# Kernel optimization log

Hardware: AMD Instinct MI355X
Metric: run time of the kernel (lower is better)

## Reference

```python
import jax, jax.numpy as jnp
import numpy as np
from jax import lax

DIM = 192
HEADS = 8
B, H, W = 8, 128, 128


def dwconv3x3(x, w):
    # x: [B,C,H,W], w: [C,1,3,3] depthwise (groups=C)
    return lax.conv_general_dilated(
        x, w, window_strides=(1, 1), padding='SAME',
        feature_group_count=x.shape[1],
        dimension_numbers=('NCHW', 'OIHW', 'NCHW'))


def conv1x1(x, w, b=None):
    # w: [Cout, Cin]
    y = jnp.einsum('oc,bchw->bohw', w, x)
    if b is not None:
        y = y + b[None, :, None, None]
    return y


def setup_inputs() -> dict:
    key = jax.random.key(0)
    ks = jax.random.split(key, 9)
    s = 0.02
    return {
        'x': jax.random.normal(ks[0], (B, DIM, H, W), jnp.float32),
        'w_qkv': jax.random.normal(ks[1], (3 * DIM, DIM), jnp.float32) * s,
        'b_qkv': jnp.zeros((3 * DIM,), jnp.float32),
        'w_dw': jax.random.normal(ks[2], (3 * DIM, 1, 3, 3), jnp.float32) * s,
        'b_dw': jnp.zeros((3 * DIM,), jnp.float32),
        'w_proj': jax.random.normal(ks[3], (DIM, DIM), jnp.float32) * s,
        'b_proj': jnp.zeros((DIM,), jnp.float32),
        'w_pos1': jax.random.normal(ks[4], (DIM, 1, 3, 3), jnp.float32) * s,
        'w_pos2': jax.random.normal(ks[5], (DIM, 1, 3, 3), jnp.float32) * s,
        'temperature': jnp.ones((HEADS, 1, 1), jnp.float32),
    }


def reference(x, w_qkv, b_qkv, w_dw, b_dw, w_proj, b_proj, w_pos1, w_pos2, temperature):
    b, c, h, w = x.shape
    heads = HEADS
    ch = c // heads

    qkv = conv1x1(x, w_qkv, b_qkv)
    qkv = dwconv3x3(qkv, w_dw) + b_dw[None, :, None, None]
    q_inp, k_inp, v_inp = jnp.split(qkv, 3, axis=1)

    def to_heads(t):  # [B,C,H,W] -> [B,heads,ch,HW]
        return t.reshape(b, heads, ch, h * w)

    q = to_heads(q_inp)
    k = to_heads(k_inp)
    v = to_heads(v_inp)

    # L2 normalize over hw (torch F.normalize, eps=1e-12)
    q = q / jnp.maximum(jnp.linalg.norm(q, axis=-1, keepdims=True), 1e-12)
    k = k / jnp.maximum(jnp.linalg.norm(k, axis=-1, keepdims=True), 1e-12)

    attn = jnp.einsum('bhce,bhde->bhcd', q, k) * temperature  # [B,heads,ch,ch]
    attn = jax.nn.softmax(attn, axis=-1)
    out = jnp.einsum('bhcd,bhde->bhce', attn, v)  # [B,heads,ch,HW]
    out = out.reshape(b, c, h, w)

    out = conv1x1(out, w_proj, b_proj)

    pos = dwconv3x3(v_inp, w_pos1)
    pos = jax.nn.gelu(pos, approximate=False)
    pos = dwconv3x3(pos, w_pos2)

    return out + pos
```

## Files before the change

### kernel.cpp

```cpp
#include <hip/hip_runtime.h>
#include <stdint.h>
#include <stddef.h>

#define NB 8
#define CC 192
#define C3 576
#define HGT 128
#define WID 128
#define HW 16384
#define NH 8
#define QKROW 49152

typedef short bf16x8 __attribute__((ext_vector_type(8)));
typedef float f32x4 __attribute__((ext_vector_type(4)));

__device__ __forceinline__ unsigned short f2bf(float f) {
  unsigned int u = __float_as_uint(f);
  u += 0x7fffu + ((u >> 16) & 1u);
  return (unsigned short)(u >> 16);
}
__device__ __forceinline__ float bf2f(unsigned short h) {
  return __uint_as_float(((unsigned int)h) << 16);
}
__device__ __forceinline__ float bflo(unsigned int v) {
  return __uint_as_float(v << 16);
}
__device__ __forceinline__ float bfhi(unsigned int v) {
  return __uint_as_float(v & 0xffff0000u);
}
__device__ __forceinline__ unsigned int pk2(float a, float b) {
  return (unsigned int)f2bf(a) | ((unsigned int)f2bf(b) << 16);
}
__device__ __forceinline__ void gl_lds16(const void* g, void* l) {
  __builtin_amdgcn_global_load_lds(
      (const __attribute__((address_space(1))) unsigned int*)(uintptr_t)g,
      (__attribute__((address_space(3))) unsigned int*)(uint32_t)(uintptr_t)l,
      16, 0, 0);
}
__device__ __forceinline__ int xcd_swz(int g, int n) {
  return (g & 7) * (n >> 3) + (g >> 3);
}

__global__ void kwprep(const float* __restrict__ wq, unsigned char* __restrict__ wb) {
  int f = blockIdx.x * 256 + threadIdx.x;
  if (f >= C3 * 24) return;
  int oc = f / 24, s = f % 24;
  unsigned int wv[4];
#pragma unroll
  for (int j = 0; j < 4; ++j)
    wv[j] = pk2(wq[oc * 192 + s * 8 + 2 * j], wq[oc * 192 + s * 8 + 2 * j + 1]);
  uint4 st; st.x = wv[0]; st.y = wv[1]; st.z = wv[2]; st.w = wv[3];
  *(uint4*)(wb + (size_t)oc * 384 + ((s ^ (oc & 7)) * 16)) = st;
}

__global__ __launch_bounds__(256) void kqkv(const float* __restrict__ x,
                                            const unsigned char* __restrict__ wb,
                                            const float* __restrict__ bqkv,
                                            unsigned short* __restrict__ vout,
                                            unsigned char* __restrict__ qkout) {
  __shared__ __align__(16) unsigned char lds[81920];
  const int ABF = 49152;
  const int TRO = 73728;
  int wg = xcd_swz(blockIdx.x, gridDim.x);
  int t = wg & 255, b = wg >> 8;
  int p0 = t * 64;
  int tid = threadIdx.x;

  const unsigned char* gx = (const unsigned char*)(x + (size_t)b * CC * HW + p0);
#pragma unroll
  for (int i = 0; i < 12; ++i) {
    int f = i * 256 + tid;
    int ch = f >> 4, seg = f & 15;
    gl_lds16(gx + ((size_t)ch * HW + seg * 4) * 4, lds + f * 16);
  }
  asm volatile("s_waitcnt vmcnt(0)" ::: "memory");
  __syncthreads();
  {
    const float* lx = (const float*)lds;
    int p = tid & 63, sg = tid >> 6;
#pragma unroll
    for (int s6 = 0; s6 < 6; ++s6) {
      int s = sg * 6 + s6;
      unsigned int wv[4];
#pragma unroll
      for (int j = 0; j < 4; ++j)
        wv[j] = pk2(lx[(s * 8 + 2 * j) * 64 + p], lx[(s * 8 + 2 * j + 1) * 64 + p]);
      uint4 st; st.x = wv[0]; st.y = wv[1]; st.z = wv[2]; st.w = wv[3];
      *(uint4*)(lds + ABF + (s * 64 + p) * 16) = st;
    }
  }
  __syncthreads();

#pragma unroll
  for (int i = 0; i < 6; ++i)
    gl_lds16(wb + i * 4096 + tid * 16, lds + i * 4096 + tid * 16);

  int lane = tid & 63, w = tid >> 6;
  int l15 = lane & 15, gq = lane >> 4;
  int pw = w * 16;
  int y = t >> 1, xh = (t & 1) * 8;
  int unitw = w * 2 + (gq >> 1);
  int sub8 = (gq & 1) * 8;
  int s4 = w * 4 + gq;
  int ru = tid >> 5, rc0 = tid & 31;
  int vc = tid >> 2, vxq = tid & 3;

  for (int ot = 0; ot < 9; ++ot) {
    if (ot == 0) { asm volatile("s_waitcnt vmcnt(0)" ::: "memory"); }
    else         { asm volatile("s_waitcnt vmcnt(2)" ::: "memory"); }
    __builtin_amdgcn_s_barrier();
    __builtin_amdgcn_sched_barrier(0);
    int nb = ot & 1;
    float bias[4];
#pragma unroll
    for (int nf = 0; nf < 4; ++nf) bias[nf] = bqkv[ot * 64 + nf * 16 + l15];
    if (ot < 8) {
      const unsigned char* gB = wb + (size_t)(ot + 1) * 24576;
#pragma unroll
      for (int i = 0; i < 6; ++i)
        gl_lds16(gB + i * 4096 + tid * 16, lds + (nb ^ 1) * 24576 + i * 4096 + tid * 16);
    }
    f32x4 acc[4];
#pragma unroll
    for (int nf = 0; nf < 4; ++nf) acc[nf] = (f32x4){0.f, 0.f, 0.f, 0.f};
#pragma unroll
    for (int kk = 0; kk < 6; ++kk) {
      bf16x8 a = *(const bf16x8*)(lds + ABF + (((kk * 4 + gq) * 64) + pw + l15) * 16);
      int cb = kk * 64 + gq * 16;
#pragma unroll
      for (int nf = 0; nf < 4; ++nf) {
        int r = nf * 16 + l15;
        bf16x8 bfr = *(const bf16x8*)(lds + nb * 24576 + r * 384 + (cb ^ ((r & 7) << 4)));
        acc[nf] = __builtin_amdgcn_mfma_f32_16x16x32_bf16(a, bfr, acc[nf], 0, 0, 0);
      }
    }
    bool isq = (ot < 6);
    if (isq) {
#pragma unroll
      for (int nf = 0; nf < 4; ++nf) {
        int c = nf * 16 + l15;
        uint2 st;
        st.x = pk2(acc[nf][0] + bias[nf], acc[nf][1] + bias[nf]);
        st.y = pk2(acc[nf][2] + bias[nf], acc[nf][3] + bias[nf]);
        *(uint2*)(lds + TRO + c * 128 + ((unitw ^ (c & 7)) * 16) + sub8) = st;
      }
    } else {
#pragma unroll
      for (int nf = 0; nf < 4; ++nf) {
        int c = nf * 16 + l15;
        uint2 st;
        st.x = pk2(acc[nf][0] + bias[nf], acc[nf][1] + bias[nf]);
        st.y = pk2(acc[nf][2] + bias[nf], acc[nf][3] + bias[nf]);
        *(uint2*)(lds + TRO + c * 128 + ((s4 ^ (c & 15)) * 8)) = st;
      }
    }
    asm volatile("s_waitcnt lgkmcnt(0)" ::: "memory");
    __builtin_amdgcn_s_barrier();
    __builtin_amdgcn_sched_barrier(0);
    if (isq) {
      int part = ot / 3, cm0 = (ot % 3) * 64;
      int c1 = rc0 + 32;
      uint4 v0 = *(const uint4*)(lds + TRO + rc0 * 128 + ((ru ^ (rc0 & 7)) * 16));
      uint4 v1 = *(const uint4*)(lds + TRO + c1 * 128 + ((ru ^ (c1 & 7)) * 16));
      unsigned char* grow = qkout + ((size_t)((part * 8 + b) * 128 + y)) * QKROW +
                            (xh + ru) * 3072 + cm0 * 16;
      *(uint4*)(grow + rc0 * 16) = v0;
      *(uint4*)(grow + c1 * 16) = v1;
    } else {
      uint2 q0 = *(const uint2*)(lds + TRO + vc * 128 + (((4 * vxq + 0) ^ (vc & 15)) * 8));
      uint2 q1 = *(const uint2*)(lds + TRO + vc * 128 + (((4 * vxq + 1) ^ (vc & 15)) * 8));
      uint2 q2 = *(const uint2*)(lds + TRO + vc * 128 + (((4 * vxq + 2) ^ (vc & 15)) * 8));
      uint2 q3 = *(const uint2*)(lds + TRO + vc * 128 + (((4 * vxq + 3) ^ (vc & 15)) * 8));
      unsigned short* vp = vout + ((size_t)(b * CC + (ot - 6) * 64 + vc)) * HW + p0 + vxq * 16;
      uint4 s0; s0.x = q0.x; s0.y = q0.y; s0.z = q1.x; s0.w = q1.y;
      uint4 s1; s1.x = q2.x; s1.y = q2.y; s1.z = q3.x; s1.w = q3.y;
      *(uint4*)vp = s0;
      *(uint4*)(vp + 8) = s1;
    }
  }
}

__global__ __launch_bounds__(256) void kqk(const unsigned char* __restrict__ qk,
                                           const float* __restrict__ wdw,
                                           const float* __restrict__ bdw,
                                           float* __restrict__ G,
                                           float* __restrict__ nq,
                                           float* __restrict__ nk) {
  __shared__ __align__(16) unsigned char lds[81920];
  const int FB = 49152;
  int wg = xcd_swz(blockIdx.x, gridDim.x);
  int band = wg & 63, h = (wg >> 6) & 7, b = wg >> 9;
  int y0 = band * 2;
  int tid = threadIdx.x;
#pragma unroll
  for (int i = 0; i < 12; ++i) {
    int f = i * 256 + tid;
    int p = f / 1536, rem = f % 1536;
    int r = rem / 384, unit = rem % 384;
    int uc = unit / 24, ch = unit % 24;
    int y = y0 - 1 + r;
    if (y >= 0 && y < HGT)
      gl_lds16(qk + ((size_t)((p * 8 + b) * 128 + y)) * QKROW + uc * 3072 + (h * 24 + ch) * 16,
               lds + f * 16);
    else
      *(uint4*)(lds + f * 16) = (uint4){0, 0, 0, 0};
  }
  asm volatile("s_waitcnt vmcnt(0)" ::: "memory");
  __syncthreads();

  int lane = tid & 63, w = tid >> 6;
  if (tid < 192) {
    int p = tid / 96; int r3m = tid % 96;
    int ch = r3m >> 2; int row = (r3m >> 1) & 1; int half = r3m & 1;
    int gc = p * 192 + h * 24 + ch;
    float wv[9];
#pragma unroll
    for (int j = 0; j < 9; ++j) wv[j] = wdw[gc * 9 + j];
    float bias = bdw[gc];
    const unsigned char* sbase = lds + p * 24576 + ch * 16;
    unsigned char* fb = lds + FB + p * 16384 + ch * 16;
    int h8 = half * 8;
    unsigned int W[3][16];
#define LOADU(dy_, m_, u_) { \
    uint4 tt = ((u_) >= 0 && (u_) < 16) \
        ? *(const uint4*)(sbase + (row + (dy_)) * 6144 + (u_) * 384) \
        : (uint4){0, 0, 0, 0}; \
    W[dy_][(m_) * 4 + 0] = tt.x; W[dy_][(m_) * 4 + 1] = tt.y; \
    W[dy_][(m_) * 4 + 2] = tt.z; W[dy_][(m_) * 4 + 3] = tt.w; }
#pragma unroll
    for (int dy = 0; dy < 3; ++dy) {
#pragma unroll
      for (int m = 0; m < 4; ++m) { LOADU(dy, m, h8 - 1 + m); }
    }
    float nsum = 0.f;
#pragma unroll
    for (int c4 = 0; c4 < 4; ++c4) {
      if (c4 > 0) {
#pragma unroll
        for (int dy = 0; dy < 3; ++dy) {
#pragma unroll
          for (int e = 0; e < 8; ++e) W[dy][e] = W[dy][8 + e];
          LOADU(dy, 2, h8 - 1 + c4 * 2 + 2);
          LOADU(dy, 3, h8 - 1 + c4 * 2 + 3);
        }
      }
      float acc[16];
#pragma unroll
      for (int j = 0; j < 16; ++j) acc[j] = bias;
#pragma unroll
      for (int dy = 0; dy < 3; ++dy) {
        float f[18];
#pragma unroll
        for (int t2 = 0; t2 < 18; ++t2) {
          int rel = 7 + t2;
          unsigned int v = W[dy][rel >> 1];
          f[t2] = (rel & 1) ? bfhi(v) : bflo(v);
        }
#pragma unroll
        for (int j = 0; j < 16; ++j)
          acc[j] += f[j] * wv[dy * 3] + f[j + 1] * wv[dy * 3 + 1] + f[j + 2] * wv[dy * 3 + 2];
      }
#pragma unroll
      for (int j = 0; j < 16; ++j) nsum += acc[j] * acc[j];
      unsigned int pk[8];
#pragma unroll
      for (int e = 0; e < 8; ++e) pk[e] = pk2(acc[2 * e], acc[2 * e + 1]);
      int kt = row * 4 + half * 2 + (c4 >> 1);
      int gb = (c4 & 1) * 2;
      uint4 s0; s0.x = pk[0]; s0.y = pk[1]; s0.z = pk[2]; s0.w = pk[3];
      uint4 s1; s1.x = pk[4]; s1.y = pk[5]; s1.z = pk[6]; s1.w = pk[7];
      *(uint4*)(fb + kt * 2048 + gb * 512) = s0;
      *(uint4*)(fb + kt * 2048 + (gb + 1) * 512) = s1;
    }
#undef LOADU
    nsum += __shfl_xor(nsum, 1);
    nsum += __shfl_xor(nsum, 2);
    if ((tid & 3) == 0) {
      float* dst = (p == 0) ? nq : nk;
      atomicAdd(dst + (b * NH + h) * 24 + ch, nsum);
    }
  } else {
    int t2 = tid - 192;
#pragma unroll
    for (int i = 0; i < 8; ++i) {
      int f = i * 64 + t2;
      int ch8 = f & 7, gq4 = (f >> 3) & 3, kt8 = (f >> 5) & 7, pp = f >> 8;
      *(uint4*)(lds + FB + pp * 16384 + kt8 * 2048 + gq4 * 512 + (24 + ch8) * 16) =
          (uint4){0, 0, 0, 0};
    }
  }
  __syncthreads();

  int l15 = lane & 15, gq = lane >> 4;
  f32x4 acc2[2][2];
#pragma unroll
  for (int ct = 0; ct < 2; ++ct)
#pragma unroll
    for (int dt = 0; dt < 2; ++dt) acc2[ct][dt] = (f32x4){0.f, 0.f, 0.f, 0.f};
#pragma unroll
  for (int t2 = 0; t2 < 2; ++t2) {
    int kt = w * 2 + t2;
    bf16x8 aq[2], bk[2];
#pragma unroll
    for (int ct = 0; ct < 2; ++ct) {
      aq[ct] = *(const bf16x8*)(lds + FB + kt * 2048 + gq * 512 + (ct * 16 + l15) * 16);
      bk[ct] = *(const bf16x8*)(lds + FB + 16384 + kt * 2048 + gq * 512 + (ct * 16 + l15) * 16);
    }
#pragma unroll
    for (int ct = 0; ct < 2; ++ct)
#pragma unroll
      for (int dt = 0; dt < 2; ++dt)
        acc2[ct][dt] = __builtin_amdgcn_mfma_f32_16x16x32_bf16(aq[ct], bk[dt], acc2[ct][dt], 0, 0, 0);
  }
  float* gp = (float*)lds;
#pragma unroll
  for (int ct = 0; ct < 2; ++ct)
#pragma unroll
    for (int dt = 0; dt < 2; ++dt)
      *(f32x4*)(gp + (((w * 4 + ct * 2 + dt) * 64) + lane) * 4) = acc2[ct][dt];
  __syncthreads();
  float* Gb = G + (size_t)(b * NH + h) * 576;
#pragma unroll
  for (int ii = 0; ii < 3; ++ii) {
    int f = ii * 256 + tid;
    if (f < 576) {
      int c = f / 24, d = f % 24;
      int t4 = ((c >> 4) << 1) + (d >> 4);
      int lane16 = (d & 15) + (((c & 15) >> 2) << 4);
      int reg = c & 3;
      float s = 0.f;
#pragma unroll
      for (int w4 = 0; w4 < 4; ++w4)
        s += gp[((w4 * 4 + t4) * 64 + lane16) * 4 + reg];
      atomicAdd(Gb + f, s);
    }
  }
}

__global__ __launch_bounds__(256) void kdwv(const unsigned short* __restrict__ src,
                                            const float* __restrict__ wdw,
                                            const float* __restrict__ bdw,
                                            unsigned char* __restrict__ vT) {
  __shared__ __align__(16) unsigned int smem[8 * 721];
  int wg = xcd_swz(blockIdx.x, gridDim.x);
  int cg = wg % 24, rt = (wg / 24) & 15, b = wg / 384;
  int y0 = rt * 8, chg0 = cg * 8;
  int tid = threadIdx.x;
  for (int i = tid; i < 5768; i += 256) smem[i] = 0;
  __syncthreads();
#pragma unroll
  for (int i = 0; i < 5; ++i) {
    int f = i * 256 + tid;
    int ch = f / 160, rem = f % 160;
    int r = rem >> 4, seg = rem & 15;
    int y = y0 - 1 + r;
    if (y >= 0 && y < HGT) {
      uint4 v = *(const uint4*)(src + ((size_t)(b * CC + chg0 + ch)) * HW + y * WID + seg * 8);
      unsigned int* dp = smem + ch * 721 + r * 72 + 4 + seg * 4;
      dp[0] = v.x; dp[1] = v.y; dp[2] = v.z; dp[3] = v.w;
    }
  }
  __syncthreads();
  int ch = tid >> 5, u = tid & 31;
  int row = u >> 2, xs = (u & 3) * 32;
  int gch = 384 + chg0 + ch;
  float wv[9];
#pragma unroll
  for (int j = 0; j < 9; ++j) wv[j] = wdw[gch * 9 + j];
  float bias = bdw[gch];
  float outv[32];
  const unsigned int* tb = smem + ch * 721;
#pragma unroll
  for (int g = 0; g < 4; ++g) {
    int x0 = xs + g * 8;
    float v[3][12];
#pragma unroll
    for (int dy = 0; dy < 3; ++dy) {
      const unsigned int* rp = tb + (row + dy) * 72 + ((x0 + 6) >> 1);
#pragma unroll
      for (int m = 0; m < 6; ++m) {
        unsigned int w2 = rp[m];
        v[dy][2 * m] = bf2f((unsigned short)(w2 & 0xffff));
        v[dy][2 * m + 1] = bf2f((unsigned short)(w2 >> 16));
      }
    }
#pragma unroll
    for (int j = 0; j < 8; ++j) {
      float a = bias;
#pragma unroll
      for (int dy = 0; dy < 3; ++dy)
#pragma unroll
        for (int dx = 0; dx < 3; ++dx)
          a += v[dy][j + dx + 1] * wv[dy * 3 + dx];
      outv[g * 8 + j] = a;
    }
  }
  __syncthreads();
  unsigned short* vt = (unsigned short*)smem;
#pragma unroll
  for (int g = 0; g < 4; ++g)
#pragma unroll
    for (int j = 0; j < 8; j += 2) {
      int x = xs + g * 8 + j;
      ((unsigned int*)smem)[ch * 512 + row * 64 + (x >> 1)] =
          pk2(outv[g * 8 + j], outv[g * 8 + j + 1]);
    }
  __syncthreads();
#pragma unroll
  for (int i = 0; i < 4; ++i) {
    int f = i * 256 + tid;
    int r = f >> 7, col = f & 127;
    unsigned int wvp[4];
#pragma unroll
    for (int e = 0; e < 4; ++e) {
      unsigned short a = vt[(2 * e) * 1024 + r * 128 + col];
      unsigned short bb = vt[(2 * e + 1) * 1024 + r * 128 + col];
      wvp[e] = (unsigned int)a | ((unsigned int)bb << 16);
    }
    uint4 st; st.x = wvp[0]; st.y = wvp[1]; st.z = wvp[2]; st.w = wvp[3];
    *(uint4*)(vT + (((size_t)(b * 24 + cg)) * HW + (size_t)(y0 + r) * WID + col) * 16) = st;
  }
}

__global__ __launch_bounds__(256) void kattn(const float* __restrict__ G,
                                             const float* __restrict__ nq,
                                             const float* __restrict__ nk,
                                             const float* __restrict__ temp,
                                             const float* __restrict__ wproj,
                                             unsigned char* __restrict__ W2) {
  __shared__ float attn[24][24];
  __shared__ float iq[24], ik[24];
  int bh = blockIdx.x;
  int h = bh & 7, b = bh >> 3;
  int tid = threadIdx.x;
  const float* Gb = G + (size_t)bh * 576;
  if (tid < 24) { float n = sqrtf(nq[bh * 24 + tid]); iq[tid] = 1.f / fmaxf(n, 1e-12f); }
  else if (tid < 48) { float n = sqrtf(nk[bh * 24 + tid - 24]); ik[tid - 24] = 1.f / fmaxf(n, 1e-12f); }
  __syncthreads();
  if (tid < 24) {
    float tmp = temp[h];
    float row[24];
    float mx = -1e30f;
#pragma unroll
    for (int d = 0; d < 24; ++d) {
      row[d] = Gb[tid * 24 + d] * iq[tid] * ik[d] * tmp;
      mx = fmaxf(mx, row[d]);
    }
    float sum = 0.f;
#pragma unroll
    for (int d = 0; d < 24; ++d) { float e = expf(row[d] - mx); row[d] = e; sum += e; }
    float inv = 1.f / sum;
#pragma unroll
    for (int d = 0; d < 24; ++d) attn[tid][d] = row[d] * inv;
  }
  __syncthreads();
  for (int i = 0; i < 18; ++i) {
    int f = tid + i * 256;
    if (f >= 4608) break;
    int oc = f / 24, d = f % 24;
    float s = 0.f;
#pragma unroll
    for (int c = 0; c < 24; ++c) s += wproj[oc * 192 + h * 24 + c] * attn[c][d];
    int gg = h * 24 + d;
    *(unsigned short*)(W2 + ((size_t)b * CC + oc) * 384 + ((gg * 2) ^ ((oc & 7) << 4))) = f2bf(s);
  }
}

__global__ __launch_bounds__(256) void kpos(const unsigned char* __restrict__ vT,
                                            const float* __restrict__ w1,
                                            const float* __restrict__ w2,
                                            unsigned short* __restrict__ pos) {
  __shared__ unsigned int vbuf[8 * 865];
  __shared__ unsigned int d1[8 * 721];
  int wg = xcd_swz(blockIdx.x, gridDim.x);
  int cg = wg % 24, rt = (wg / 24) & 15, b = wg / 384;
  int y0 = rt * 8, g0 = cg * 8;
  int tid = threadIdx.x;
  for (int i = tid; i < 6920; i += 256) vbuf[i] = 0;
  __syncthreads();
#pragma unroll
  for (int i = 0; i < 3; ++i) {
    int f = i * 256 + tid;
    int r = f >> 6, colp = f & 63;
    int y = y0 - 2 + r;
    if (y >= 0 && y < HGT) {
      const unsigned char* base = vT + (((size_t)(b * 24 + cg)) * HW + (size_t)y * WID + colp * 2) * 16;
      uint4 va = *(const uint4*)(base);
      uint4 vb2 = *(const uint4*)(base + 16);
      unsigned int la[4] = {va.x, va.y, va.z, va.w};
      unsigned int lb[4] = {vb2.x, vb2.y, vb2.z, vb2.w};
#pragma unroll
      for (int e = 0; e < 8; ++e) {
        unsigned int a16 = (la[e >> 1] >> ((e & 1) * 16)) & 0xffff;
        unsigned int b16 = (lb[e >> 1] >> ((e & 1) * 16)) & 0xffff;
        vbuf[e * 865 + r * 72 + colp + 4] = a16 | (b16 << 16);
      }
    }
  }
  __syncthreads();
  int ch = tid >> 5, u = tid & 31;
  {
    const float* wp = w1 + (g0 + ch) * 9;
    float wl[9];
#pragma unroll
    for (int j = 0; j < 9; ++j) wl[j] = wp[j];
    int x0 = u * 4;
    for (int rr = 0; rr < 10; ++rr) {
      int y = y0 - 1 + rr;
      unsigned int o0 = 0, o1 = 0;
      if (y >= 0 && y < HGT) {
        float v[3][8];
#pragma unroll
        for (int dy = 0; dy < 3; ++dy) {
          const unsigned int* rp = vbuf + ch * 865 + (rr + dy) * 72 + ((x0 + 6) >> 1);
#pragma unroll
          for (int m = 0; m < 4; ++m) {
            unsigned int w2r = rp[m];
            v[dy][2 * m] = bf2f((unsigned short)(w2r & 0xffff));
            v[dy][2 * m + 1] = bf2f((unsigned short)(w2r >> 16));
          }
        }
        float g4[4];
#pragma unroll
        for (int j = 0; j < 4; ++j) {
          float a = 0.f;
#pragma unroll
          for (int dy = 0; dy < 3; ++dy)
#pragma unroll
            for (int dx = 0; dx < 3; ++dx)
              a += v[dy][j + dx + 1] * wl[dy * 3 + dx];
          g4[j] = 0.5f * a * (1.f + erff(a * 0.70710678118f));
        }
        o0 = pk2(g4[0], g4[1]);
        o1 = pk2(g4[2], g4[3]);
      }
      unsigned int* dp = d1 + ch * 721 + rr * 72 + ((x0 + 8) >> 1);
      dp[0] = o0; dp[1] = o1;
    }
  }
  if (tid < 160) {
    int ech = tid / 20, rem = tid % 20;
    int rr = rem >> 1, side = rem & 1;
    int x = side ? 128 : -1;
    int y = y0 - 1 + rr;
    unsigned short val = 0;
    if (y >= 0 && y < HGT) {
      const float* wp = w1 + (g0 + ech) * 9;
      float a = 0.f;
      const unsigned short* vb16 = (const unsigned short*)(vbuf + ech * 865);
#pragma unroll
      for (int dy = 0; dy < 3; ++dy)
#pragma unroll
        for (int dx = 0; dx < 3; ++dx)
          a += bf2f(vb16[(rr + dy) * 144 + (x + dx + 7)]) * wp[dy * 3 + dx];
      val = f2bf(0.5f * a * (1.f + erff(a * 0.70710678118f)));
    }
    ((unsigned short*)(d1 + ech * 721))[rr * 144 + (x + 8)] = val;
  }
  __syncthreads();
  {
    const float* wp = w2 + (g0 + ch) * 9;
    float wl[9];
#pragma unroll
    for (int j = 0; j < 9; ++j) wl[j] = wp[j];
    int row = u >> 2, xs = (u & 3) * 32;
    size_t rb = ((size_t)(b * CC + g0 + ch)) * HW + (size_t)(y0 + row) * WID;
#pragma unroll
    for (int g = 0; g < 4; ++g) {
      int x0 = xs + g * 8;
      float v[3][12];
#pragma unroll
      for (int dy = 0; dy < 3; ++dy) {
        const unsigned int* rp = d1 + ch * 721 + (row + dy) * 72 + ((x0 + 6) >> 1);
#pragma unroll
        for (int m = 0; m < 6; ++m) {
          unsigned int w2r = rp[m];
          v[dy][2 * m] = bf2f((unsigned short)(w2r & 0xffff));
          v[dy][2 * m + 1] = bf2f((unsigned short)(w2r >> 16));
        }
      }
      uint4 st;
      float o[8];
#pragma unroll
      for (int j = 0; j < 8; ++j) {
        float a = 0.f;
#pragma unroll
        for (int dy = 0; dy < 3; ++dy)
#pragma unroll
          for (int dx = 0; dx < 3; ++dx)
            a += v[dy][j + dx + 1] * wl[dy * 3 + dx];
        o[j] = a;
      }
      st.x = pk2(o[0], o[1]); st.y = pk2(o[2], o[3]);
      st.z = pk2(o[4], o[5]); st.w = pk2(o[6], o[7]);
      *(uint4*)(pos + rb + x0) = st;
    }
  }
}

__global__ __launch_bounds__(256) void kproj(const unsigned char* __restrict__ vT,
                                             const unsigned char* __restrict__ W2,
                                             const float* __restrict__ bproj,
                                             const unsigned short* __restrict__ pos,
                                             float* __restrict__ out) {
  __shared__ __align__(16) unsigned char lds[73728];
  int wg = xcd_swz(blockIdx.x, gridDim.x);
  int ot = wg % 3; int rest = wg / 3; int grp = rest & 63; int b = rest >> 6;
  int tid = threadIdx.x;
  const unsigned char* gB = W2 + ((size_t)(b * 192 + ot * 64)) * 384;
#pragma unroll
  for (int i = 0; i < 6; ++i)
    gl_lds16(gB + i * 4096 + tid * 16, lds + 49152 + i * 4096 + tid * 16);
  const unsigned char* gA = vT + (size_t)b * 24 * HW * 16;
  int t0 = grp * 4;
  {
    int p0 = t0 * 64;
#pragma unroll
    for (int i = 0; i < 6; ++i) {
      int f = i * 256 + tid;
      gl_lds16(gA + (((size_t)(f >> 6)) * HW + p0 + (f & 63)) * 16, lds + f * 16);
    }
  }
  int lane = tid & 63, w = tid >> 6;
  int l15 = lane & 15, gq = lane >> 4;
  int pw = w * 16;
  float bias[4];
  size_t obase[4];
#pragma unroll
  for (int nf = 0; nf < 4; ++nf) {
    int oc = ot * 64 + nf * 16 + l15;
    bias[nf] = bproj[oc];
    obase[nf] = ((size_t)(b * 192 + oc)) * HW;
  }
  for (int it = 0; it < 4; ++it) {
    int tile = t0 + it;
    asm volatile("s_waitcnt vmcnt(0)" ::: "memory");
    __syncthreads();
    int nb = it & 1;
    if (it < 3) {
      int p1 = (tile + 1) * 64;
#pragma unroll
      for (int i = 0; i < 6; ++i) {
        int f = i * 256 + tid;
        gl_lds16(gA + (((size_t)(f >> 6)) * HW + p1 + (f & 63)) * 16,
                 lds + ((nb ^ 1) * 24576) + f * 16);
      }
    }
    f32x4 acc[4];
#pragma unroll
    for (int nf = 0; nf < 4; ++nf) acc[nf] = (f32x4){0.f, 0.f, 0.f, 0.f};
#pragma unroll
    for (int kk = 0; kk < 6; ++kk) {
      bf16x8 a = *(const bf16x8*)(lds + nb * 24576 + ((((kk * 4 + gq) << 6) + pw + l15) * 16));
      int cb = kk * 64 + gq * 16;
#pragma unroll
      for (int nf = 0; nf < 4; ++nf) {
        int r = nf * 16 + l15;
        bf16x8 bfr = *(const bf16x8*)(lds + 49152 + r * 384 + (cb ^ ((r & 7) << 4)));
        acc[nf] = __builtin_amdgcn_mfma_f32_16x16x32_bf16(a, bfr, acc[nf], 0, 0, 0);
      }
    }
    int p = tile * 64 + pw + gq * 4;
#pragma unroll
    for (int nf = 0; nf < 4; ++nf) {
      uint2 pv = *(const uint2*)(pos + obase[nf] + p);
      float4 o;
      o.x = acc[nf][0] + bias[nf] + bf2f((unsigned short)(pv.x & 0xffff));
      o.y = acc[nf][1] + bias[nf] + bf2f((unsigned short)(pv.x >> 16));
      o.z = acc[nf][2] + bias[nf] + bf2f((unsigned short)(pv.y & 0xffff));
      o.w = acc[nf][3] + bias[nf] + bf2f((unsigned short)(pv.y >> 16));
      *(float4*)(out + obase[nf] + p) = o;
    }
  }
}

#define OFF_W   ((size_t)0)
#define OFF_G   ((size_t)221184)
#define OFF_NQ  ((size_t)368640)
#define OFF_NK  ((size_t)374784)
#define OFF_W2  ((size_t)380928)
#define OFF_QK  ((size_t)970752)
#define OFF_V   ((size_t)101634048)
#define OFF_XT  ((size_t)151965696)

extern "C" void kernel_launch(void* const* d_in, const int* in_sizes, int n_in,
                              void* d_out, int out_size, void* d_ws, size_t ws_size,
                              hipStream_t stream) {
  const float* x     = (const float*)d_in[0];
  const float* wqkv  = (const float*)d_in[1];
  const float* bqkv  = (const float*)d_in[2];
  const float* wdw   = (const float*)d_in[3];
  const float* bdw   = (const float*)d_in[4];
  const float* wproj = (const float*)d_in[5];
  const float* bproj = (const float*)d_in[6];
  const float* wpos1 = (const float*)d_in[7];
  const float* wpos2 = (const float*)d_in[8];
  const float* temp  = (const float*)d_in[9];
  unsigned char* ws = (unsigned char*)d_ws;

  hipMemsetAsync(ws + OFF_G, 0, 147456 + 6144 + 6144, stream);
  kwprep<<<54, 256, 0, stream>>>(wqkv, ws + OFF_W);
  kqkv<<<2048, 256, 0, stream>>>(x, ws + OFF_W, bqkv,
                                 (unsigned short*)(ws + OFF_V), ws + OFF_QK);
  kqk<<<4096, 256, 0, stream>>>(ws + OFF_QK, wdw, bdw, (float*)(ws + OFF_G),
                                (float*)(ws + OFF_NQ), (float*)(ws + OFF_NK));
  kdwv<<<3072, 256, 0, stream>>>((const unsigned short*)(ws + OFF_V), wdw, bdw,
                                 ws + OFF_XT);
  kattn<<<64, 256, 0, stream>>>((const float*)(ws + OFF_G), (const float*)(ws + OFF_NQ),
                                (const float*)(ws + OFF_NK), temp, wproj, ws + OFF_W2);
  kpos<<<3072, 256, 0, stream>>>(ws + OFF_XT, wpos1, wpos2,
                                 (unsigned short*)(ws + OFF_QK));
  kproj<<<1536, 256, 0, stream>>>(ws + OFF_XT, ws + OFF_W2, bproj,
                                  (const unsigned short*)(ws + OFF_QK), (float*)d_out);
}
```

Baseline: 289.3 us.

## Fuse V depthwise conv with positional convs and pipeline QKV GEMM stores

Merges the V depthwise conv kernel and the positional dwconv-GELU-dwconv kernel into one kernel, which recomputes V's dwconv on a 2-row halo so pos can be computed without re-reading vT from global memory. This removes a launch and a global round trip of the V activations. The QKV GEMM kernel now prefetches weight tiles into registers instead of direct-to-LDS loads, caches the bias in LDS, and double-buffers the transpose staging so each tile's global store overlaps the next tile's MFMA work. The tradeoffs are extra halo compute, more LDS per block in the fused kernel, and higher register pressure in the GEMM.

```diff
diff --git a/kernel.cpp b/kernel.cpp
--- a/kernel.cpp
+++ b/kernel.cpp
@@ -58,9 +58,12 @@
                                             const float* __restrict__ bqkv,
                                             unsigned short* __restrict__ vout,
                                             unsigned char* __restrict__ qkout) {
-  __shared__ __align__(16) unsigned char lds[81920];
-  const int ABF = 49152;
-  const int TRO = 73728;
+  __shared__ __align__(16) unsigned char lds[73728];
+  const int ABF = 0;
+  const int TRO = 24576;
+  const int BIAS = 40960;
+  const int BB = 43264;
+  const int STG = 24576;
   int wg = xcd_swz(blockIdx.x, gridDim.x);
   int t = wg & 255, b = wg >> 8;
   int p0 = t * 64;
@@ -71,12 +74,22 @@
   for (int i = 0; i < 12; ++i) {
     int f = i * 256 + tid;
     int ch = f >> 4, seg = f & 15;
-    gl_lds16(gx + ((size_t)ch * HW + seg * 4) * 4, lds + f * 16);
+    gl_lds16(gx + ((size_t)ch * HW + seg * 4) * 4, lds + STG + f * 16);
+  }
+  uint4 breg[2][6];
+#pragma unroll
+  for (int i = 0; i < 6; ++i)
+    breg[0][i] = *(const uint4*)(wb + i * 4096 + tid * 16);
+  float bsr[3];
+#pragma unroll
+  for (int i = 0; i < 3; ++i) {
+    int f = i * 256 + tid;
+    bsr[i] = (f < 576) ? bqkv[f] : 0.f;
   }
   asm volatile("s_waitcnt vmcnt(0)" ::: "memory");
   __syncthreads();
   {
-    const float* lx = (const float*)lds;
+    const float* lx = (const float*)(lds + STG);
     int p = tid & 63, sg = tid >> 6;
 #pragma unroll
     for (int s6 = 0; s6 < 6; ++s6) {
@@ -90,10 +103,11 @@
     }
   }
   __syncthreads();
-
-#pragma unroll
-  for (int i = 0; i < 6; ++i)
-    gl_lds16(wb + i * 4096 + tid * 16, lds + i * 4096 + tid * 16);
+#pragma unroll
+  for (int i = 0; i < 3; ++i) {
+    int f = i * 256 + tid;
+    if (f < 576) ((float*)(lds + BIAS))[f] = bsr[i];
+  }
 
   int lane = tid & 63, w = tid >> 6;
   int l15 = lane & 15, gq = lane >> 4;
@@ -105,20 +119,23 @@
   int ru = tid >> 5, rc0 = tid & 31;
   int vc = tid >> 2, vxq = tid & 3;
 
+#pragma unroll
   for (int ot = 0; ot < 9; ++ot) {
-    if (ot == 0) { asm volatile("s_waitcnt vmcnt(0)" ::: "memory"); }
-    else         { asm volatile("s_waitcnt vmcnt(2)" ::: "memory"); }
+    int cur = ot & 1;
+    asm volatile("s_waitcnt lgkmcnt(0)" ::: "memory");
     __builtin_amdgcn_s_barrier();
     __builtin_amdgcn_sched_barrier(0);
-    int nb = ot & 1;
-    float bias[4];
-#pragma unroll
-    for (int nf = 0; nf < 4; ++nf) bias[nf] = bqkv[ot * 64 + nf * 16 + l15];
+#pragma unroll
+    for (int i = 0; i < 6; ++i)
+      *(uint4*)(lds + BB + i * 4096 + tid * 16) = breg[cur][i];
+    asm volatile("s_waitcnt lgkmcnt(0)" ::: "memory");
+    __builtin_amdgcn_s_barrier();
+    __builtin_amdgcn_sched_barrier(0);
     if (ot < 8) {
-      const unsigned char* gB = wb + (size_t)(ot + 1) * 24576;
 #pragma unroll
       for (int i = 0; i < 6; ++i)
-        gl_lds16(gB + i * 4096 + tid * 16, lds + (nb ^ 1) * 24576 + i * 4096 + tid * 16);
+        breg[cur ^ 1][i] =
+            *(const uint4*)(wb + (size_t)(ot + 1) * 24576 + i * 4096 + tid * 16);
     }
     f32x4 acc[4];
 #pragma unroll
@@ -130,19 +147,23 @@
 #pragma unroll
       for (int nf = 0; nf < 4; ++nf) {
         int r = nf * 16 + l15;
-        bf16x8 bfr = *(const bf16x8*)(lds + nb * 24576 + r * 384 + (cb ^ ((r & 7) << 4)));
+        bf16x8 bfr = *(const bf16x8*)(lds + BB + r * 384 + (cb ^ ((r & 7) << 4)));
         acc[nf] = __builtin_amdgcn_mfma_f32_16x16x32_bf16(a, bfr, acc[nf], 0, 0, 0);
       }
     }
-    bool isq = (ot < 6);
-    if (isq) {
+    float bias[4];
+#pragma unroll
+    for (int nf = 0; nf < 4; ++nf)
+      bias[nf] = ((const float*)(lds + BIAS))[ot * 64 + nf * 16 + l15];
+    unsigned char* tr = lds + TRO + cur * 8192;
+    if (ot < 6) {
 #pragma unroll
       for (int nf = 0; nf < 4; ++nf) {
         int c = nf * 16 + l15;
         uint2 st;
         st.x = pk2(acc[nf][0] + bias[nf], acc[nf][1] + bias[nf]);
         st.y = pk2(acc[nf][2] + bias[nf], acc[nf][3] + bias[nf]);
-        *(uint2*)(lds + TRO + c * 128 + ((unitw ^ (c & 7)) * 16) + sub8) = st;
+        *(uint2*)(tr + c * 128 + ((unitw ^ (c & 7)) * 16) + sub8) = st;
       }
     } else {
 #pragma unroll
@@ -151,32 +172,48 @@
         uint2 st;
         st.x = pk2(acc[nf][0] + bias[nf], acc[nf][1] + bias[nf]);
         st.y = pk2(acc[nf][2] + bias[nf], acc[nf][3] + bias[nf]);
-        *(uint2*)(lds + TRO + c * 128 + ((s4 ^ (c & 15)) * 8)) = st;
-      }
-    }
-    asm volatile("s_waitcnt lgkmcnt(0)" ::: "memory");
-    __builtin_amdgcn_s_barrier();
-    __builtin_amdgcn_sched_barrier(0);
-    if (isq) {
-      int part = ot / 3, cm0 = (ot % 3) * 64;
-      int c1 = rc0 + 32;
-      uint4 v0 = *(const uint4*)(lds + TRO + rc0 * 128 + ((ru ^ (rc0 & 7)) * 16));
-      uint4 v1 = *(const uint4*)(lds + TRO + c1 * 128 + ((ru ^ (c1 & 7)) * 16));
-      unsigned char* grow = qkout + ((size_t)((part * 8 + b) * 128 + y)) * QKROW +
-                            (xh + ru) * 3072 + cm0 * 16;
-      *(uint4*)(grow + rc0 * 16) = v0;
-      *(uint4*)(grow + c1 * 16) = v1;
-    } else {
-      uint2 q0 = *(const uint2*)(lds + TRO + vc * 128 + (((4 * vxq + 0) ^ (vc & 15)) * 8));
-      uint2 q1 = *(const uint2*)(lds + TRO + vc * 128 + (((4 * vxq + 1) ^ (vc & 15)) * 8));
-      uint2 q2 = *(const uint2*)(lds + TRO + vc * 128 + (((4 * vxq + 2) ^ (vc & 15)) * 8));
-      uint2 q3 = *(const uint2*)(lds + TRO + vc * 128 + (((4 * vxq + 3) ^ (vc & 15)) * 8));
-      unsigned short* vp = vout + ((size_t)(b * CC + (ot - 6) * 64 + vc)) * HW + p0 + vxq * 16;
-      uint4 s0; s0.x = q0.x; s0.y = q0.y; s0.z = q1.x; s0.w = q1.y;
-      uint4 s1; s1.x = q2.x; s1.y = q2.y; s1.z = q3.x; s1.w = q3.y;
-      *(uint4*)vp = s0;
-      *(uint4*)(vp + 8) = s1;
-    }
+        *(uint2*)(tr + c * 128 + ((s4 ^ (c & 15)) * 8)) = st;
+      }
+    }
+    if (ot > 0) {
+      int j = ot - 1;
+      unsigned char* trp = lds + TRO + (cur ^ 1) * 8192;
+      if (j < 6) {
+        int part = j / 3, cm0 = (j % 3) * 64;
+        int c1 = rc0 + 32;
+        uint4 v0 = *(const uint4*)(trp + rc0 * 128 + ((ru ^ (rc0 & 7)) * 16));
+        uint4 v1 = *(const uint4*)(trp + c1 * 128 + ((ru ^ (c1 & 7)) * 16));
+        unsigned char* grow = qkout + ((size_t)((part * 8 + b) * 128 + y)) * QKROW +
+                              (xh + ru) * 3072 + cm0 * 16;
+        *(uint4*)(grow + rc0 * 16) = v0;
+        *(uint4*)(grow + c1 * 16) = v1;
+      } else {
+        uint2 q0 = *(const uint2*)(trp + vc * 128 + (((4 * vxq + 0) ^ (vc & 15)) * 8));
+        uint2 q1 = *(const uint2*)(trp + vc * 128 + (((4 * vxq + 1) ^ (vc & 15)) * 8));
+        uint2 q2 = *(const uint2*)(trp + vc * 128 + (((4 * vxq + 2) ^ (vc & 15)) * 8));
+        uint2 q3 = *(const uint2*)(trp + vc * 128 + (((4 * vxq + 3) ^ (vc & 15)) * 8));
+        unsigned short* vp = vout + ((size_t)(b * CC + (j - 6) * 64 + vc)) * HW + p0 + vxq * 16;
+        uint4 s0; s0.x = q0.x; s0.y = q0.y; s0.z = q1.x; s0.w = q1.y;
+        uint4 s1; s1.x = q2.x; s1.y = q2.y; s1.z = q3.x; s1.w = q3.y;
+        *(uint4*)vp = s0;
+        *(uint4*)(vp + 8) = s1;
+      }
+    }
+  }
+  asm volatile("s_waitcnt lgkmcnt(0)" ::: "memory");
+  __builtin_amdgcn_s_barrier();
+  __builtin_amdgcn_sched_barrier(0);
+  {
+    unsigned char* trp = lds + TRO;
+    uint2 q0 = *(const uint2*)(trp + vc * 128 + (((4 * vxq + 0) ^ (vc & 15)) * 8));
+    uint2 q1 = *(const uint2*)(trp + vc * 128 + (((4 * vxq + 1) ^ (vc & 15)) * 8));
+    uint2 q2 = *(const uint2*)(trp + vc * 128 + (((4 * vxq + 2) ^ (vc & 15)) * 8));
+    uint2 q3 = *(const uint2*)(trp + vc * 128 + (((4 * vxq + 3) ^ (vc & 15)) * 8));
+    unsigned short* vp = vout + ((size_t)(b * CC + 2 * 64 + vc)) * HW + p0 + vxq * 16;
+    uint4 s0; s0.x = q0.x; s0.y = q0.y; s0.z = q1.x; s0.w = q1.y;
+    uint4 s1; s1.x = q2.x; s1.y = q2.y; s1.z = q3.x; s1.w = q3.y;
+    *(uint4*)vp = s0;
+    *(uint4*)(vp + 8) = s1;
   }
 }
 
@@ -337,74 +374,78 @@
   }
 }
 
-__global__ __launch_bounds__(256) void kdwv(const unsigned short* __restrict__ src,
-                                            const float* __restrict__ wdw,
-                                            const float* __restrict__ bdw,
-                                            unsigned char* __restrict__ vT) {
-  __shared__ __align__(16) unsigned int smem[8 * 721];
+__global__ __launch_bounds__(256) void kvpos(const unsigned short* __restrict__ vsrc,
+                                             const float* __restrict__ wdw,
+                                             const float* __restrict__ bdw,
+                                             const float* __restrict__ w1,
+                                             const float* __restrict__ w2,
+                                             unsigned char* __restrict__ vT,
+                                             unsigned short* __restrict__ pos) {
+  __shared__ __align__(16) unsigned int smem[14992];
+  const int VP = 6920;
   int wg = xcd_swz(blockIdx.x, gridDim.x);
   int cg = wg % 24, rt = (wg / 24) & 15, b = wg / 384;
-  int y0 = rt * 8, chg0 = cg * 8;
+  int y0 = rt * 8, g0 = cg * 8;
   int tid = threadIdx.x;
-  for (int i = tid; i < 5768; i += 256) smem[i] = 0;
-  __syncthreads();
-#pragma unroll
-  for (int i = 0; i < 5; ++i) {
+  for (int i = tid; i < 14992; i += 256) smem[i] = 0;
+  __syncthreads();
+#pragma unroll
+  for (int i = 0; i < 7; ++i) {
     int f = i * 256 + tid;
-    int ch = f / 160, rem = f % 160;
+    int ch = f / 224, rem = f % 224;
     int r = rem >> 4, seg = rem & 15;
-    int y = y0 - 1 + r;
+    int y = y0 - 3 + r;
     if (y >= 0 && y < HGT) {
-      uint4 v = *(const uint4*)(src + ((size_t)(b * CC + chg0 + ch)) * HW + y * WID + seg * 8);
-      unsigned int* dp = smem + ch * 721 + r * 72 + 4 + seg * 4;
+      uint4 v = *(const uint4*)(vsrc + ((size_t)(b * CC + g0 + ch)) * HW + y * WID + seg * 8);
+      unsigned int* dp = smem + VP + ch * 1009 + r * 72 + 4 + seg * 4;
       dp[0] = v.x; dp[1] = v.y; dp[2] = v.z; dp[3] = v.w;
     }
   }
   __syncthreads();
-  int ch = tid >> 5, u = tid & 31;
-  int row = u >> 2, xs = (u & 3) * 32;
-  int gch = 384 + chg0 + ch;
-  float wv[9];
-#pragma unroll
-  for (int j = 0; j < 9; ++j) wv[j] = wdw[gch * 9 + j];
-  float bias = bdw[gch];
-  float outv[32];
-  const unsigned int* tb = smem + ch * 721;
-#pragma unroll
-  for (int g = 0; g < 4; ++g) {
-    int x0 = xs + g * 8;
-    float v[3][12];
-#pragma unroll
-    for (int dy = 0; dy < 3; ++dy) {
-      const unsigned int* rp = tb + (row + dy) * 72 + ((x0 + 6) >> 1);
-#pragma unroll
-      for (int m = 0; m < 6; ++m) {
-        unsigned int w2 = rp[m];
-        v[dy][2 * m] = bf2f((unsigned short)(w2 & 0xffff));
-        v[dy][2 * m + 1] = bf2f((unsigned short)(w2 >> 16));
-      }
-    }
-#pragma unroll
-    for (int j = 0; j < 8; ++j) {
-      float a = bias;
-#pragma unroll
-      for (int dy = 0; dy < 3; ++dy)
-#pragma unroll
-        for (int dx = 0; dx < 3; ++dx)
-          a += v[dy][j + dx + 1] * wv[dy * 3 + dx];
-      outv[g * 8 + j] = a;
-    }
-  }
-  __syncthreads();
-  unsigned short* vt = (unsigned short*)smem;
-#pragma unroll
-  for (int g = 0; g < 4; ++g)
-#pragma unroll
-    for (int j = 0; j < 8; j += 2) {
-      int x = xs + g * 8 + j;
-      ((unsigned int*)smem)[ch * 512 + row * 64 + (x >> 1)] =
-          pk2(outv[g * 8 + j], outv[g * 8 + j + 1]);
-    }
+  {
+    int ch = tid >> 5, u = tid & 31;
+    int gch = 384 + g0 + ch;
+    float wv[9];
+#pragma unroll
+    for (int j = 0; j < 9; ++j) wv[j] = wdw[gch * 9 + j];
+    float bias = bdw[gch];
+    const unsigned int* tb = smem + VP + ch * 1009;
+    unsigned int* ob = smem + ch * 865;
+#pragma unroll
+    for (int i = 0; i < 6; ++i) {
+      int s = u + i * 32;
+      int row = s >> 4, seg = s & 15;
+      int y = y0 - 2 + row;
+      if (y >= 0 && y < HGT) {
+        int x0 = seg * 8;
+        float v[3][12];
+#pragma unroll
+        for (int dy = 0; dy < 3; ++dy) {
+          const unsigned int* rp = tb + (row + dy) * 72 + ((x0 + 6) >> 1);
+#pragma unroll
+          for (int m = 0; m < 6; ++m) {
+            unsigned int w2r = rp[m];
+            v[dy][2 * m] = bflo(w2r);
+            v[dy][2 * m + 1] = bfhi(w2r);
+          }
+        }
+        float o[8];
+#pragma unroll
+        for (int j = 0; j < 8; ++j) {
+          float a = bias;
+#pragma unroll
+          for (int dy = 0; dy < 3; ++dy)
+#pragma unroll
+            for (int dx = 0; dx < 3; ++dx)
+              a += v[dy][j + dx + 1] * wv[dy * 3 + dx];
+          o[j] = a;
+        }
+        unsigned int* dp = ob + row * 72 + 4 + seg * 4;
+        dp[0] = pk2(o[0], o[1]); dp[1] = pk2(o[2], o[3]);
+        dp[2] = pk2(o[4], o[5]); dp[3] = pk2(o[6], o[7]);
+      }
+    }
+  }
   __syncthreads();
 #pragma unroll
   for (int i = 0; i < 4; ++i) {
@@ -413,12 +454,111 @@
     unsigned int wvp[4];
 #pragma unroll
     for (int e = 0; e < 4; ++e) {
-      unsigned short a = vt[(2 * e) * 1024 + r * 128 + col];
-      unsigned short bb = vt[(2 * e + 1) * 1024 + r * 128 + col];
+      unsigned short a = ((const unsigned short*)(smem + (2 * e) * 865))[(r + 2) * 144 + 8 + col];
+      unsigned short bb = ((const unsigned short*)(smem + (2 * e + 1) * 865))[(r + 2) * 144 + 8 + col];
       wvp[e] = (unsigned int)a | ((unsigned int)bb << 16);
     }
     uint4 st; st.x = wvp[0]; st.y = wvp[1]; st.z = wvp[2]; st.w = wvp[3];
     *(uint4*)(vT + (((size_t)(b * 24 + cg)) * HW + (size_t)(y0 + r) * WID + col) * 16) = st;
+  }
+  unsigned int* d1 = smem + VP;
+  int ch = tid >> 5, u = tid & 31;
+  {
+    const float* wp = w1 + (g0 + ch) * 9;
+    float wl[9];
+#pragma unroll
+    for (int j = 0; j < 9; ++j) wl[j] = wp[j];
+    int x0 = u * 4;
+    for (int rr = 0; rr < 10; ++rr) {
+      int y = y0 - 1 + rr;
+      unsigned int o0 = 0, o1 = 0;
+      if (y >= 0 && y < HGT) {
+        float v[3][8];
+#pragma unroll
+        for (int dy = 0; dy < 3; ++dy) {
+          const unsigned int* rp = smem + ch * 865 + (rr + dy) * 72 + ((x0 + 6) >> 1);
+#pragma unroll
+          for (int m = 0; m < 4; ++m) {
+            unsigned int w2r = rp[m];
+            v[dy][2 * m] = bflo(w2r);
+            v[dy][2 * m + 1] = bfhi(w2r);
+          }
+        }
+        float g4[4];
+#pragma unroll
+        for (int j = 0; j < 4; ++j) {
+          float a = 0.f;
+#pragma unroll
+          for (int dy = 0; dy < 3; ++dy)
+#pragma unroll
+            for (int dx = 0; dx < 3; ++dx)
+              a += v[dy][j + dx + 1] * wl[dy * 3 + dx];
+          g4[j] = 0.5f * a * (1.f + erff(a * 0.70710678118f));
+        }
+        o0 = pk2(g4[0], g4[1]);
+        o1 = pk2(g4[2], g4[3]);
+      }
+      unsigned int* dp = d1 + ch * 721 + rr * 72 + ((x0 + 8) >> 1);
+      dp[0] = o0; dp[1] = o1;
+    }
+  }
+  if (tid < 160) {
+    int ech = tid / 20, rem = tid % 20;
+    int rr = rem >> 1, side = rem & 1;
+    int x = side ? 128 : -1;
+    int y = y0 - 1 + rr;
+    unsigned short val = 0;
+    if (y >= 0 && y < HGT) {
+      const float* wp = w1 + (g0 + ech) * 9;
+      float a = 0.f;
+      const unsigned short* vb16 = (const unsigned short*)(smem + ech * 865);
+#pragma unroll
+      for (int dy = 0; dy < 3; ++dy)
+#pragma unroll
+        for (int dx = 0; dx < 3; ++dx)
+          a += bf2f(vb16[(rr + dy) * 144 + (x + dx + 7)]) * wp[dy * 3 + dx];
+      val = f2bf(0.5f * a * (1.f + erff(a * 0.70710678118f)));
+    }
+    ((unsigned short*)(d1 + ech * 721))[rr * 144 + (x + 8)] = val;
+  }
+  __syncthreads();
+  {
+    const float* wp = w2 + (g0 + ch) * 9;
+    float wl[9];
+#pragma unroll
+    for (int j = 0; j < 9; ++j) wl[j] = wp[j];
+    int row = u >> 2, xs = (u & 3) * 32;
+    size_t rb = ((size_t)(b * CC + g0 + ch)) * HW + (size_t)(y0 + row) * WID;
+#pragma unroll
+    for (int g = 0; g < 4; ++g) {
+      int x0 = xs + g * 8;
+      float v[3][12];
+#pragma unroll
+      for (int dy = 0; dy < 3; ++dy) {
+        const unsigned int* rp = d1 + ch * 721 + (row + dy) * 72 + ((x0 + 6) >> 1);
+#pragma unroll
+        for (int m = 0; m < 6; ++m) {
+          unsigned int w2r = rp[m];
+          v[dy][2 * m] = bflo(w2r);
+          v[dy][2 * m + 1] = bfhi(w2r);
+        }
+      }
+      uint4 st;
+      float o[8];
+#pragma unroll
+      for (int j = 0; j < 8; ++j) {
+        float a = 0.f;
+#pragma unroll
+        for (int dy = 0; dy < 3; ++dy)
+#pragma unroll
+          for (int dx = 0; dx < 3; ++dx)
+            a += v[dy][j + dx + 1] * wl[dy * 3 + dx];
+        o[j] = a;
+      }
+      st.x = pk2(o[0], o[1]); st.y = pk2(o[2], o[3]);
+      st.z = pk2(o[4], o[5]); st.w = pk2(o[6], o[7]);
+      *(uint4*)(pos + rb + x0) = st;
+    }
   }
 }
 
@@ -466,138 +606,6 @@
   }
 }
 
-__global__ __launch_bounds__(256) void kpos(const unsigned char* __restrict__ vT,
-                                            const float* __restrict__ w1,
-                                            const float* __restrict__ w2,
-                                            unsigned short* __restrict__ pos) {
-  __shared__ unsigned int vbuf[8 * 865];
-  __shared__ unsigned int d1[8 * 721];
-  int wg = xcd_swz(blockIdx.x, gridDim.x);
-  int cg = wg % 24, rt = (wg / 24) & 15, b = wg / 384;
-  int y0 = rt * 8, g0 = cg * 8;
-  int tid = threadIdx.x;
-  for (int i = tid; i < 6920; i += 256) vbuf[i] = 0;
-  __syncthreads();
-#pragma unroll
-  for (int i = 0; i < 3; ++i) {
-    int f = i * 256 + tid;
-    int r = f >> 6, colp = f & 63;
-    int y = y0 - 2 + r;
-    if (y >= 0 && y < HGT) {
-      const unsigned char* base = vT + (((size_t)(b * 24 + cg)) * HW + (size_t)y * WID + colp * 2) * 16;
-      uint4 va = *(const uint4*)(base);
-      uint4 vb2 = *(const uint4*)(base + 16);
-      unsigned int la[4] = {va.x, va.y, va.z, va.w};
-      unsigned int lb[4] = {vb2.x, vb2.y, vb2.z, vb2.w};
-#pragma unroll
-      for (int e = 0; e < 8; ++e) {
-        unsigned int a16 = (la[e >> 1] >> ((e & 1) * 16)) & 0xffff;
-        unsigned int b16 = (lb[e >> 1] >> ((e & 1) * 16)) & 0xffff;
-        vbuf[e * 865 + r * 72 + colp + 4] = a16 | (b16 << 16);
-      }
-    }
-  }
-  __syncthreads();
-  int ch = tid >> 5, u = tid & 31;
-  {
-    const float* wp = w1 + (g0 + ch) * 9;
-    float wl[9];
-#pragma unroll
-    for (int j = 0; j < 9; ++j) wl[j] = wp[j];
-    int x0 = u * 4;
-    for (int rr = 0; rr < 10; ++rr) {
-      int y = y0 - 1 + rr;
-      unsigned int o0 = 0, o1 = 0;
-      if (y >= 0 && y < HGT) {
-        float v[3][8];
-#pragma unroll
-        for (int dy = 0; dy < 3; ++dy) {
-          const unsigned int* rp = vbuf + ch * 865 + (rr + dy) * 72 + ((x0 + 6) >> 1);
-#pragma unroll
-          for (int m = 0; m < 4; ++m) {
-            unsigned int w2r = rp[m];
-            v[dy][2 * m] = bf2f((unsigned short)(w2r & 0xffff));
-            v[dy][2 * m + 1] = bf2f((unsigned short)(w2r >> 16));
-          }
-        }
-        float g4[4];
-#pragma unroll
-        for (int j = 0; j < 4; ++j) {
-          float a = 0.f;
-#pragma unroll
-          for (int dy = 0; dy < 3; ++dy)
-#pragma unroll
-            for (int dx = 0; dx < 3; ++dx)
-              a += v[dy][j + dx + 1] * wl[dy * 3 + dx];
-          g4[j] = 0.5f * a * (1.f + erff(a * 0.70710678118f));
-        }
-        o0 = pk2(g4[0], g4[1]);
-        o1 = pk2(g4[2], g4[3]);
-      }
-      unsigned int* dp = d1 + ch * 721 + rr * 72 + ((x0 + 8) >> 1);
-      dp[0] = o0; dp[1] = o1;
-    }
-  }
-  if (tid < 160) {
-    int ech = tid / 20, rem = tid % 20;
-    int rr = rem >> 1, side = rem & 1;
-    int x = side ? 128 : -1;
-    int y = y0 - 1 + rr;
-    unsigned short val = 0;
-    if (y >= 0 && y < HGT) {
-      const float* wp = w1 + (g0 + ech) * 9;
-      float a = 0.f;
-      const unsigned short* vb16 = (const unsigned short*)(vbuf + ech * 865);
-#pragma unroll
-      for (int dy = 0; dy < 3; ++dy)
-#pragma unroll
-        for (int dx = 0; dx < 3; ++dx)
-          a += bf2f(vb16[(rr + dy) * 144 + (x + dx + 7)]) * wp[dy * 3 + dx];
-      val = f2bf(0.5f * a * (1.f + erff(a * 0.70710678118f)));
-    }
-    ((unsigned short*)(d1 + ech * 721))[rr * 144 + (x + 8)] = val;
-  }
-  __syncthreads();
-  {
-    const float* wp = w2 + (g0 + ch) * 9;
-    float wl[9];
-#pragma unroll
-    for (int j = 0; j < 9; ++j) wl[j] = wp[j];
-    int row = u >> 2, xs = (u & 3) * 32;
-    size_t rb = ((size_t)(b * CC + g0 + ch)) * HW + (size_t)(y0 + row) * WID;
-#pragma unroll
-    for (int g = 0; g < 4; ++g) {
-      int x0 = xs + g * 8;
-      float v[3][12];
-#pragma unroll
-      for (int dy = 0; dy < 3; ++dy) {
-        const unsigned int* rp = d1 + ch * 721 + (row + dy) * 72 + ((x0 + 6) >> 1);
-#pragma unroll
-        for (int m = 0; m < 6; ++m) {
-          unsigned int w2r = rp[m];
-          v[dy][2 * m] = bf2f((unsigned short)(w2r & 0xffff));
-          v[dy][2 * m + 1] = bf2f((unsigned short)(w2r >> 16));
-        }
-      }
-      uint4 st;
-      float o[8];
-#pragma unroll
-      for (int j = 0; j < 8; ++j) {
-        float a = 0.f;
-#pragma unroll
-        for (int dy = 0; dy < 3; ++dy)
-#pragma unroll
-          for (int dx = 0; dx < 3; ++dx)
-            a += v[dy][j + dx + 1] * wl[dy * 3 + dx];
-        o[j] = a;
-      }
-      st.x = pk2(o[0], o[1]); st.y = pk2(o[2], o[3]);
-      st.z = pk2(o[4], o[5]); st.w = pk2(o[6], o[7]);
-      *(uint4*)(pos + rb + x0) = st;
-    }
-  }
-}
-
 __global__ __launch_bounds__(256) void kproj(const unsigned char* __restrict__ vT,
                                              const unsigned char* __restrict__ W2,
                                              const float* __restrict__ bproj,
@@ -704,12 +712,11 @@
                                  (unsigned short*)(ws + OFF_V), ws + OFF_QK);
   kqk<<<4096, 256, 0, stream>>>(ws + OFF_QK, wdw, bdw, (float*)(ws + OFF_G),
                                 (float*)(ws + OFF_NQ), (float*)(ws + OFF_NK));
-  kdwv<<<3072, 256, 0, stream>>>((const unsigned short*)(ws + OFF_V), wdw, bdw,
-                                 ws + OFF_XT);
+  kvpos<<<3072, 256, 0, stream>>>((const unsigned short*)(ws + OFF_V), wdw, bdw,
+                                  wpos1, wpos2, ws + OFF_XT,
+                                  (unsigned short*)(ws + OFF_QK));
   kattn<<<64, 256, 0, stream>>>((const float*)(ws + OFF_G), (const float*)(ws + OFF_NQ),
                                 (const float*)(ws + OFF_NK), temp, wproj, ws + OFF_W2);
-  kpos<<<3072, 256, 0, stream>>>(ws + OFF_XT, wpos1, wpos2,
-                                 (unsigned short*)(ws + OFF_QK));
   kproj<<<1536, 256, 0, stream>>>(ws + OFF_XT, ws + OFF_W2, bproj,
                                   (const unsigned short*)(ws + OFF_QK), (float*)d_out);
 }
```

Result: slower. 434.0 us (+50.0%).
